# Optimization experiments

Measured on AMD Instinct MI355X. Metric: run time of the kernel, lower is better.

## Reference

```python
import jax, jax.numpy as jnp
import numpy as np

L = 32768      # sequence length
D_MODEL = 256  # input/output feature dim
D_HIDDEN = 256 # diagonal recurrent state dim
R_MIN, R_MAX, MAX_PHASE = 0.0, 1.0, 6.28


def setup_inputs() -> dict:
    key = jax.random.key(0)
    ks = jax.random.split(key, 8)
    inputs = jax.random.normal(ks[0], (L, D_MODEL), dtype=jnp.float32)
    # nu_init: log(-0.5*log(u*(r_max^2-r_min^2)+r_min^2))
    u1 = jax.random.uniform(ks[1], (D_HIDDEN,), dtype=jnp.float32)
    nu_log = jnp.log(-0.5 * jnp.log(u1 * (R_MAX**2 - R_MIN**2) + R_MIN**2))
    # theta_init: log(max_phase*u)
    u2 = jax.random.uniform(ks[2], (D_HIDDEN,), dtype=jnp.float32)
    theta_log = jnp.log(MAX_PHASE * u2)
    # gamma_log_init from (nu_log, theta_log)
    diag_lambda = jnp.exp(-jnp.exp(nu_log) + 1j * jnp.exp(theta_log))
    gamma_log = jnp.log(jnp.sqrt(1.0 - jnp.abs(diag_lambda) ** 2))
    bnorm = np.sqrt(2 * D_MODEL).astype(np.float32) if False else jnp.sqrt(2.0 * D_MODEL)
    cnorm = jnp.sqrt(2.0 * D_HIDDEN)
    B_re = jax.random.normal(ks[3], (D_HIDDEN, D_MODEL), dtype=jnp.float32) / bnorm
    B_im = jax.random.normal(ks[4], (D_HIDDEN, D_MODEL), dtype=jnp.float32) / bnorm
    C_re = jax.random.normal(ks[5], (D_MODEL, D_HIDDEN), dtype=jnp.float32) / cnorm
    C_im = jax.random.normal(ks[6], (D_MODEL, D_HIDDEN), dtype=jnp.float32) / cnorm
    D = jax.random.normal(ks[7], (D_MODEL,), dtype=jnp.float32)
    return {"inputs": inputs, "nu_log": nu_log, "theta_log": theta_log,
            "gamma_log": gamma_log, "B_re": B_re, "B_im": B_im,
            "C_re": C_re, "C_im": C_im, "D": D}


def _binop(q_i, q_j):
    # elementwise diagonal linear-recurrence combine
    A_i, b_i = q_i
    A_j, b_j = q_j
    return (A_j * A_i, A_j * b_i + b_j)


def reference(inputs, nu_log, theta_log, gamma_log, B_re, B_im, C_re, C_im, D):
    # h_{t+1} = lambda * h_t + B_norm x_{t+1};  y_t = Re[C h_t] + D * x_t
    diag_lambda = jnp.exp(-jnp.exp(nu_log) + 1j * jnp.exp(theta_log))  # (H,)
    B_norm = (B_re + 1j * B_im) * jnp.exp(gamma_log)[:, None]          # (H, M)
    C = C_re + 1j * C_im                                               # (M, H)
    Bu = inputs.astype(B_norm.dtype) @ B_norm.T                        # (L, H) complex
    Lam = jnp.broadcast_to(diag_lambda, (inputs.shape[0], diag_lambda.shape[0]))
    _, h = jax.lax.associative_scan(_binop, (Lam, Bu))                 # (L, H)
    return jnp.real(h @ C.T) + inputs * D                              # (L, M)
```

## Files before the change

kernel.cpp:

```cpp
#include <hip/hip_runtime.h>
#include <hip/hip_bf16.h>
#include <math.h>

#define LSEQ 32768
#define DMODEL 256
#define DHID 256
#define NCH 512
#define CHUNK 128
#define NCHUNKS (LSEQ / CHUNK)

typedef __bf16 bf16_t;
typedef _Float16 f16_t;
typedef __bf16 bf16x8 __attribute__((ext_vector_type(8)));
typedef float f32x4 __attribute__((ext_vector_type(4)));

__device__ __forceinline__ void async_load16(const void* g, void* l) {
  __builtin_amdgcn_global_load_lds((__attribute__((address_space(1))) void*)g,
                                   (__attribute__((address_space(3))) void*)l,
                                   16, 0, 0);
}

__device__ __forceinline__ float f16tof(unsigned int u) {
  return (float)__builtin_bit_cast(_Float16, (unsigned short)(u & 0xffffu));
}
__device__ __forceinline__ unsigned int fTobf(float f) {
  return (unsigned int)__builtin_bit_cast(unsigned short, (bf16_t)f);
}

__global__ void prep_all(const float* __restrict__ nu_log,
                         const float* __restrict__ theta_log,
                         const float* __restrict__ gamma_log,
                         const float* __restrict__ B_re, const float* __restrict__ B_im,
                         const float* __restrict__ C_re, const float* __restrict__ C_im,
                         float* __restrict__ lam, bf16_t* __restrict__ W1,
                         bf16_t* __restrict__ W2) {
  const int bid = blockIdx.x, tid = threadIdx.x;
  if (bid < 10) {
    int h = tid;
    if (h < DHID) {
      double nu = exp((double)nu_log[h]);
      double th = exp((double)theta_log[h]);
      int row; double n;
      if (bid == 0)      { row = 0; n = 1.0; }
      else if (bid == 1) { row = 2; n = 32.0; }
      else               { row = 4 + 2 * (bid - 2); n = 128.0 * (double)(1 << (bid - 2)); }
      double mag = exp(-n * nu);
      double ph  = fmod(n * th, 6.283185307179586);
      lam[row * DHID + h]       = (float)(mag * cos(ph));
      lam[(row + 1) * DHID + h] = (float)(mag * sin(ph));
    }
  } else if (bid < 522) {
    int n = bid - 10, k = tid, h = n >> 1;
    float g = expf(gamma_log[h]);
    float v = (((n & 1) == 0) ? B_re[h * DMODEL + k] : B_im[h * DMODEL + k]) * g;
    W1[n * DMODEL + k] = (bf16_t)v;
  } else {
    int idx = bid - 522;
    int m = idx >> 1, k = (idx & 1) * 256 + tid, h = k >> 1;
    float v = ((k & 1) == 0) ? C_re[m * DHID + h] : -C_im[m * DHID + h];
    W2[m * NCH + k] = (bf16_t)v;
  }
}

__global__ __launch_bounds__(512, 4) void gemm1_scan(
    const float* __restrict__ X, const bf16_t* __restrict__ Bw,
    f16_t* __restrict__ Bu, const float* __restrict__ lam,
    float* __restrict__ E) {
  __shared__ __align__(16) char smem[69632];
  char*  Bt = smem;
  float* Ep = (float*)(smem + 65536);

  const int tid = threadIdx.x;
  const int gx = blockIdx.x;
  const int c  = blockIdx.y;
  const int r0 = c * CHUNK;
  const int c0 = gx * 256;
  const int wave = tid >> 6, lane = tid & 63;
  const int wm = wave & 1, wn = wave >> 1;
  const int lrow = lane & 15, lk = lane >> 4;
  const int ra = tid >> 2, ka = (tid & 3) * 8;

  f32x4 acc[4][4] = {};

  {
    const float* xrow = X + (size_t)(r0 + ra) * DMODEL + ka;
    float4 a0 = ((const float4*)xrow)[0];
    float4 a1 = ((const float4*)xrow)[1];
    async_load16(Bw + (size_t)(c0 + ra) * DMODEL + ka, smem + 8192 + tid * 16);
    async_load16(Bw + (size_t)(c0 + 128 + ra) * DMODEL + ka, smem + 16384 + tid * 16);
    bf16x8 av = {(bf16_t)a0.x, (bf16_t)a0.y, (bf16_t)a0.z, (bf16_t)a0.w,
                 (bf16_t)a1.x, (bf16_t)a1.y, (bf16_t)a1.z, (bf16_t)a1.w};
    *(bf16x8*)(smem + ra * 64 + ka * 2) = av;
  }
  asm volatile("s_waitcnt vmcnt(0) lgkmcnt(0)" ::: "memory");
  __builtin_amdgcn_s_barrier();

#pragma unroll
  for (int t = 0; t < 8; ++t) {
    const int cur = t & 1, nxt = cur ^ 1;
    const char* Asc = smem + cur * 24576;
    const char* Bsc = smem + 8192 + cur * 24576;
    float4 a0, a1;
    if (t < 7) {
      const int k0n = (t + 1) * 32;
      const float* xrow = X + (size_t)(r0 + ra) * DMODEL + k0n + ka;
      a0 = ((const float4*)xrow)[0];
      a1 = ((const float4*)xrow)[1];
      async_load16(Bw + (size_t)(c0 + ra) * DMODEL + k0n + ka,
                   smem + 8192 + nxt * 24576 + tid * 16);
      async_load16(Bw + (size_t)(c0 + 128 + ra) * DMODEL + k0n + ka,
                   smem + 16384 + nxt * 24576 + tid * 16);
    }
    bf16x8 af[4], bfr[4];
#pragma unroll
    for (int i = 0; i < 4; ++i)
      af[i] = *(const bf16x8*)(Asc + (wm * 64 + i * 16 + lrow) * 64 + lk * 16);
#pragma unroll
    for (int j = 0; j < 4; ++j)
      bfr[j] = *(const bf16x8*)(Bsc + (wn * 64 + j * 16 + lrow) * 64 + lk * 16);
#pragma unroll
    for (int i = 0; i < 4; ++i)
#pragma unroll
      for (int j = 0; j < 4; ++j)
        acc[i][j] = __builtin_amdgcn_mfma_f32_16x16x32_bf16(af[i], bfr[j], acc[i][j], 0, 0, 0);
    if (t < 7) {
      bf16x8 av = {(bf16_t)a0.x, (bf16_t)a0.y, (bf16_t)a0.z, (bf16_t)a0.w,
                   (bf16_t)a1.x, (bf16_t)a1.y, (bf16_t)a1.z, (bf16_t)a1.w};
      *(bf16x8*)(smem + nxt * 24576 + ra * 64 + ka * 2) = av;
    }
    asm volatile("s_waitcnt vmcnt(0) lgkmcnt(0)" ::: "memory");
    __builtin_amdgcn_s_barrier();
  }

#pragma unroll
  for (int i = 0; i < 4; ++i)
#pragma unroll
    for (int r = 0; r < 4; ++r) {
      int row = wm * 64 + i * 16 + lk * 4 + r;
      int key = (row & 7) << 4;
#pragma unroll
      for (int j = 0; j < 4; ++j) {
        int col = wn * 64 + j * 16 + lrow;
        *(f16_t*)(Bt + row * 512 + ((col * 2) ^ key)) = (f16_t)acc[i][j][r];
      }
    }
  __syncthreads();

  char* dst = (char*)Bu + (size_t)r0 * 1024 + gx * 512;
#pragma unroll
  for (int it = 0; it < 8; ++it) {
    int idx = it * 512 + tid;
    int row = idx >> 5, off = (idx & 31) * 16;
    *(f32x4*)(dst + (size_t)row * 1024 + off) = *(const f32x4*)(Bt + row * 512 + off);
  }

  {
    int p = tid & 127, seg = tid >> 7;
    int h = gx * 128 + p;
    float lre = lam[h], lim = lam[DHID + h];
    float sre = 0.f, sim = 0.f;
    int cb = 4 * p;
#pragma unroll 4
    for (int t = 0; t < 32; ++t) {
      int row = seg * 32 + t;
      unsigned int w = *(const unsigned int*)(Bt + row * 512 + (cb ^ ((row & 7) << 4)));
      float bre = f16tof(w), bim = f16tof(w >> 16);
      float nre = fmaf(lre, sre, fmaf(-lim, sim, bre));
      float nim = fmaf(lre, sim, fmaf(lim, sre, bim));
      sre = nre; sim = nim;
    }
    Ep[seg * 256 + 2 * p]     = sre;
    Ep[seg * 256 + 2 * p + 1] = sim;
  }
  __syncthreads();
  if (tid < 128) {
    int p = tid, h = gx * 128 + p;
    float ar = lam[2 * DHID + h], ai = lam[3 * DHID + h];
    float er = Ep[2 * p], ei = Ep[2 * p + 1];
#pragma unroll
    for (int s = 1; s < 4; ++s) {
      float tr = fmaf(ar, er, fmaf(-ai, ei, Ep[s * 256 + 2 * p]));
      float ti = fmaf(ar, ei, fmaf(ai, er, Ep[s * 256 + 2 * p + 1]));
      er = tr; ei = ti;
    }
    E[(size_t)c * NCH + 2 * h]     = er;
    E[(size_t)c * NCH + 2 * h + 1] = ei;
  }
}

__global__ __launch_bounds__(1024) void scan_gemm2(
    const f16_t* __restrict__ Bu, const bf16_t* __restrict__ W2,
    const float* __restrict__ lam, const float* __restrict__ E,
    const float* __restrict__ X, const float* __restrict__ Dv,
    float* __restrict__ out) {
  __shared__ __align__(16) char smem[155648];
  char*   H  = smem;
  bf16_t* Bs = (bf16_t*)(smem + 131072);
  float*  LB = (float*)(smem + 131072);
  float*  Pp = (float*)(smem + 135168);
  float*  Tt = (float*)(smem + 147456);

  const int tid = threadIdx.x;
  const int c = (int)gridDim.x - 1 - (int)blockIdx.x;
  const int r0 = c * CHUNK;

  const char* src = (const char*)Bu + (size_t)r0 * 1024;
#pragma unroll
  for (int it = 0; it < 8; ++it)
    async_load16(src + it * 16384 + tid * 16, H + it * 16384 + tid * 16);

  const char* w2src = (const char*)W2 + (size_t)(tid >> 2) * (NCH * 2) + (tid & 3) * 16;
  f32x4 wreg[2];
  wreg[0] = *(const f32x4*)(w2src);

  if (tid < 512) {
    int p = tid & 255, half = tid >> 8;
    int m = c >> 1;
    int lo = half ? m : 0, end = half ? c : m;
    float aR = lam[4 * DHID + p], aI = lam[5 * DHID + p];
    float sr = 0.f, si = 0.f;
#pragma unroll 4
    for (int k = lo; k < end; ++k) {
      float2 e = *(const float2*)(E + (size_t)k * NCH + 2 * p);
      float nr = fmaf(aR, sr, fmaf(-aI, si, e.x));
      float ni = fmaf(aR, si, fmaf(aI, sr, e.y));
      sr = nr; si = ni;
    }
    LB[half * 512 + 2 * p]     = sr;
    LB[half * 512 + 2 * p + 1] = si;
  }
  __syncthreads();

  {
    int p = tid & 255, seg = tid >> 8;
    float lre = lam[p], lim = lam[DHID + p];
    float sre = 0.f, sim = 0.f;
    int cb = 4 * p;
#pragma unroll 4
    for (int t = 0; t < 32; ++t) {
      int row = seg * 32 + t;
      unsigned int w = *(const unsigned int*)(H + row * 1024 + (cb ^ ((row & 7) << 4)));
      float bre = f16tof(w), bim = f16tof(w >> 16);
      float nre = fmaf(lre, sre, fmaf(-lim, sim, bre));
      float nim = fmaf(lre, sim, fmaf(lim, sre, bim));
      sre = nre; sim = nim;
    }
    Pp[seg * 512 + 2 * p]     = sre;
    Pp[seg * 512 + 2 * p + 1] = sim;
  }
  __syncthreads();

  if (tid < 256) {
    int p = tid;
    int lenb = c - (c >> 1);
    float pr = 1.f, pi = 0.f;
#pragma unroll
    for (int j = 0; j < 8; ++j)
      if (lenb & (1 << j)) {
        float br = lam[(4 + 2 * j) * DHID + p], bi = lam[(5 + 2 * j) * DHID + p];
        float nr = pr * br - pi * bi, ni = pr * bi + pi * br;
        pr = nr; pi = ni;
      }
    float sar = LB[2 * p], sai = LB[2 * p + 1];
    float sbr = LB[512 + 2 * p], sbi = LB[512 + 2 * p + 1];
    float tr = fmaf(pr, sar, fmaf(-pi, sai, sbr));
    float ti = fmaf(pr, sai, fmaf(pi, sar, sbi));
    float l32r = lam[2 * DHID + p], l32i = lam[3 * DHID + p];
    Tt[2 * p] = tr; Tt[2 * p + 1] = ti;
#pragma unroll
    for (int s = 1; s < 4; ++s) {
      float pR = Pp[(s - 1) * 512 + 2 * p], pI = Pp[(s - 1) * 512 + 2 * p + 1];
      float nr = fmaf(l32r, tr, fmaf(-l32i, ti, pR));
      float ni = fmaf(l32r, ti, fmaf(l32i, tr, pI));
      tr = nr; ti = ni;
      Tt[s * 512 + 2 * p] = tr; Tt[s * 512 + 2 * p + 1] = ti;
    }
  }
  __syncthreads();

  {
    int p = tid & 255, seg = tid >> 8;
    float lre = lam[p], lim = lam[DHID + p];
    float sre = Tt[seg * 512 + 2 * p], sim = Tt[seg * 512 + 2 * p + 1];
    int cb = 4 * p;
#pragma unroll 4
    for (int t = 0; t < 32; ++t) {
      int row = seg * 32 + t;
      unsigned int* ptr = (unsigned int*)(H + row * 1024 + (cb ^ ((row & 7) << 4)));
      unsigned int w = *ptr;
      float bre = f16tof(w), bim = f16tof(w >> 16);
      float nre = fmaf(lre, sre, fmaf(-lim, sim, bre));
      float nim = fmaf(lre, sim, fmaf(lim, sre, bim));
      sre = nre; sim = nim;
      *ptr = (fTobf(sim) << 16) | fTobf(sre);
    }
  }
  __syncthreads();

  const int wave = tid >> 6, lane = tid & 63;
  const int wm = wave & 3, wn = wave >> 2;
  const int lrow = lane & 15, lk = lane >> 4;
  *(f32x4*)((char*)Bs + tid * 16) = wreg[0];
  wreg[1] = *(const f32x4*)(w2src + 64);
  asm volatile("s_waitcnt lgkmcnt(0)" ::: "memory");
  __builtin_amdgcn_s_barrier();

  f32x4 acc[2][4] = {};
#pragma unroll
  for (int t = 0; t < 16; ++t) {
    const int k0 = t * 32;
    bf16x8 af[2], bfr[4];
#pragma unroll
    for (int i = 0; i < 2; ++i) {
      int m = wm * 32 + i * 16 + lrow;
      af[i] = *(const bf16x8*)(H + m * 1024 + ((2 * k0 + lk * 16) ^ ((m & 7) << 4)));
    }
#pragma unroll
    for (int j = 0; j < 4; ++j)
      bfr[j] = *(const bf16x8*)(Bs + (wn * 64 + j * 16 + lrow) * 32 + lk * 8);
#pragma unroll
    for (int i = 0; i < 2; ++i)
#pragma unroll
      for (int j = 0; j < 4; ++j)
        acc[i][j] = __builtin_amdgcn_mfma_f32_16x16x32_bf16(af[i], bfr[j], acc[i][j], 0, 0, 0);
    if (t < 15) {
      __builtin_amdgcn_s_barrier();
      *(f32x4*)((char*)Bs + tid * 16) = wreg[(t + 1) & 1];
      if (t < 14) wreg[t & 1] = *(const f32x4*)(w2src + 64 * (t + 2));
      asm volatile("s_waitcnt lgkmcnt(0)" ::: "memory");
      __builtin_amdgcn_s_barrier();
    }
  }

#pragma unroll
  for (int i = 0; i < 2; ++i)
#pragma unroll
    for (int r = 0; r < 4; ++r) {
      int row = r0 + wm * 32 + i * 16 + lk * 4 + r;
#pragma unroll
      for (int j = 0; j < 4; ++j) {
        int col = wn * 64 + j * 16 + lrow;
        float v = acc[i][j][r] + X[(size_t)row * DMODEL + col] * Dv[col];
        out[(size_t)row * DMODEL + col] = v;
      }
    }
}

extern "C" void kernel_launch(void* const* d_in, const int* in_sizes, int n_in,
                              void* d_out, int out_size, void* d_ws, size_t ws_size,
                              hipStream_t stream) {
  const float* inputs    = (const float*)d_in[0];
  const float* nu_log    = (const float*)d_in[1];
  const float* theta_log = (const float*)d_in[2];
  const float* gamma_log = (const float*)d_in[3];
  const float* B_re      = (const float*)d_in[4];
  const float* B_im      = (const float*)d_in[5];
  const float* C_re      = (const float*)d_in[6];
  const float* C_im      = (const float*)d_in[7];
  const float* Dvec      = (const float*)d_in[8];
  float* out = (float*)d_out;

  char* w = (char*)d_ws;
  bf16_t* W1 = (bf16_t*)w; w += (size_t)NCH * DMODEL * 2;
  bf16_t* W2 = (bf16_t*)w; w += (size_t)DMODEL * NCH * 2;
  float* lam = (float*)w;  w += 24576;
  f16_t* Bu  = (f16_t*)w;  w += (size_t)LSEQ * NCH * 2;
  float* E   = (float*)w;  w += (size_t)NCHUNKS * NCH * 4;

  prep_all<<<1034, 256, 0, stream>>>(nu_log, theta_log, gamma_log,
                                     B_re, B_im, C_re, C_im,
                                     lam, W1, W2);
  gemm1_scan<<<dim3(2, NCHUNKS), 512, 0, stream>>>(inputs, W1, Bu, lam, E);
  scan_gemm2<<<NCHUNKS, 1024, 0, stream>>>(Bu, W2, lam, E, inputs, Dvec, out);
}
```

Before: 148.3 us.

## Triple-buffer gemm1 K loop, batch scan LDS loads, prefetch X/D in gemm2

Result: slower. 154.0 us (+3.8%).

```diff
diff --git a/kernel.cpp b/kernel.cpp
--- a/kernel.cpp
+++ b/kernel.cpp
@@ -66,9 +66,9 @@
     const float* __restrict__ X, const bf16_t* __restrict__ Bw,
     f16_t* __restrict__ Bu, const float* __restrict__ lam,
     float* __restrict__ E) {
-  __shared__ __align__(16) char smem[69632];
+  __shared__ __align__(16) char smem[77824];
   char*  Bt = smem;
-  float* Ep = (float*)(smem + 65536);
+  float* Ep = (float*)(smem + 73728);
 
   const int tid = threadIdx.x;
   const int gx = blockIdx.x;
@@ -81,35 +81,41 @@
   const int ra = tid >> 2, ka = (tid & 3) * 8;
 
   f32x4 acc[4][4] = {};
+  const float*  xbase = X + (size_t)(r0 + ra) * DMODEL + ka;
+  const bf16_t* bw0   = Bw + (size_t)(c0 + ra) * DMODEL + ka;
+  const bf16_t* bw1   = Bw + (size_t)(c0 + 128 + ra) * DMODEL + ka;
 
   {
-    const float* xrow = X + (size_t)(r0 + ra) * DMODEL + ka;
-    float4 a0 = ((const float4*)xrow)[0];
-    float4 a1 = ((const float4*)xrow)[1];
-    async_load16(Bw + (size_t)(c0 + ra) * DMODEL + ka, smem + 8192 + tid * 16);
-    async_load16(Bw + (size_t)(c0 + 128 + ra) * DMODEL + ka, smem + 16384 + tid * 16);
-    bf16x8 av = {(bf16_t)a0.x, (bf16_t)a0.y, (bf16_t)a0.z, (bf16_t)a0.w,
-                 (bf16_t)a1.x, (bf16_t)a1.y, (bf16_t)a1.z, (bf16_t)a1.w};
-    *(bf16x8*)(smem + ra * 64 + ka * 2) = av;
-  }
-  asm volatile("s_waitcnt vmcnt(0) lgkmcnt(0)" ::: "memory");
+    float4 a00 = ((const float4*)xbase)[0];
+    float4 a01 = ((const float4*)xbase)[1];
+    float4 a10 = ((const float4*)(xbase + 32))[0];
+    float4 a11 = ((const float4*)(xbase + 32))[1];
+    async_load16(bw0, smem + 8192 + tid * 16);
+    async_load16(bw1, smem + 16384 + tid * 16);
+    async_load16(bw0 + 32, smem + 24576 + 8192 + tid * 16);
+    async_load16(bw1 + 32, smem + 24576 + 16384 + tid * 16);
+    bf16x8 av0 = {(bf16_t)a00.x, (bf16_t)a00.y, (bf16_t)a00.z, (bf16_t)a00.w,
+                  (bf16_t)a01.x, (bf16_t)a01.y, (bf16_t)a01.z, (bf16_t)a01.w};
+    *(bf16x8*)(smem + ra * 64 + ka * 2) = av0;
+    bf16x8 av1 = {(bf16_t)a10.x, (bf16_t)a10.y, (bf16_t)a10.z, (bf16_t)a10.w,
+                  (bf16_t)a11.x, (bf16_t)a11.y, (bf16_t)a11.z, (bf16_t)a11.w};
+    *(bf16x8*)(smem + 24576 + ra * 64 + ka * 2) = av1;
+  }
+  asm volatile("s_waitcnt vmcnt(2) lgkmcnt(0)" ::: "memory");
   __builtin_amdgcn_s_barrier();
 
 #pragma unroll
   for (int t = 0; t < 8; ++t) {
-    const int cur = t & 1, nxt = cur ^ 1;
+    const int cur = t % 3, nx2 = (t + 2) % 3;
     const char* Asc = smem + cur * 24576;
     const char* Bsc = smem + 8192 + cur * 24576;
     float4 a0, a1;
-    if (t < 7) {
-      const int k0n = (t + 1) * 32;
-      const float* xrow = X + (size_t)(r0 + ra) * DMODEL + k0n + ka;
-      a0 = ((const float4*)xrow)[0];
-      a1 = ((const float4*)xrow)[1];
-      async_load16(Bw + (size_t)(c0 + ra) * DMODEL + k0n + ka,
-                   smem + 8192 + nxt * 24576 + tid * 16);
-      async_load16(Bw + (size_t)(c0 + 128 + ra) * DMODEL + k0n + ka,
-                   smem + 16384 + nxt * 24576 + tid * 16);
+    if (t < 6) {
+      const int k0n = (t + 2) * 32;
+      a0 = ((const float4*)(xbase + k0n))[0];
+      a1 = ((const float4*)(xbase + k0n))[1];
+      async_load16(bw0 + k0n, smem + nx2 * 24576 + 8192 + tid * 16);
+      async_load16(bw1 + k0n, smem + nx2 * 24576 + 16384 + tid * 16);
     }
     bf16x8 af[4], bfr[4];
 #pragma unroll
@@ -123,12 +129,14 @@
 #pragma unroll
       for (int j = 0; j < 4; ++j)
         acc[i][j] = __builtin_amdgcn_mfma_f32_16x16x32_bf16(af[i], bfr[j], acc[i][j], 0, 0, 0);
-    if (t < 7) {
+    if (t < 6) {
       bf16x8 av = {(bf16_t)a0.x, (bf16_t)a0.y, (bf16_t)a0.z, (bf16_t)a0.w,
                    (bf16_t)a1.x, (bf16_t)a1.y, (bf16_t)a1.z, (bf16_t)a1.w};
-      *(bf16x8*)(smem + nxt * 24576 + ra * 64 + ka * 2) = av;
-    }
-    asm volatile("s_waitcnt vmcnt(0) lgkmcnt(0)" ::: "memory");
+      *(bf16x8*)(smem + nx2 * 24576 + ra * 64 + ka * 2) = av;
+      asm volatile("s_waitcnt vmcnt(2) lgkmcnt(0)" ::: "memory");
+    } else {
+      asm volatile("s_waitcnt vmcnt(0) lgkmcnt(0)" ::: "memory");
+    }
     __builtin_amdgcn_s_barrier();
   }
 
@@ -160,14 +168,21 @@
     float lre = lam[h], lim = lam[DHID + h];
     float sre = 0.f, sim = 0.f;
     int cb = 4 * p;
-#pragma unroll 4
-    for (int t = 0; t < 32; ++t) {
-      int row = seg * 32 + t;
-      unsigned int w = *(const unsigned int*)(Bt + row * 512 + (cb ^ ((row & 7) << 4)));
-      float bre = f16tof(w), bim = f16tof(w >> 16);
-      float nre = fmaf(lre, sre, fmaf(-lim, sim, bre));
-      float nim = fmaf(lre, sim, fmaf(lim, sre, bim));
-      sre = nre; sim = nim;
+#pragma unroll
+    for (int half = 0; half < 2; ++half) {
+      unsigned int wv[16];
+#pragma unroll
+      for (int t = 0; t < 16; ++t) {
+        int row = seg * 32 + half * 16 + t;
+        wv[t] = *(const unsigned int*)(Bt + row * 512 + (cb ^ ((row & 7) << 4)));
+      }
+#pragma unroll
+      for (int t = 0; t < 16; ++t) {
+        float bre = f16tof(wv[t]), bim = f16tof(wv[t] >> 16);
+        float nre = fmaf(lre, sre, fmaf(-lim, sim, bre));
+        float nim = fmaf(lre, sim, fmaf(lim, sre, bim));
+        sre = nre; sim = nim;
+      }
     }
     Ep[seg * 256 + 2 * p]     = sre;
     Ep[seg * 256 + 2 * p + 1] = sim;
@@ -203,6 +218,9 @@
   const int tid = threadIdx.x;
   const int c = (int)gridDim.x - 1 - (int)blockIdx.x;
   const int r0 = c * CHUNK;
+  const int wave = tid >> 6, lane = tid & 63;
+  const int wm = wave & 3, wn = wave >> 2;
+  const int lrow = lane & 15, lk = lane >> 4;
 
   const char* src = (const char*)Bu + (size_t)r0 * 1024;
 #pragma unroll
@@ -212,6 +230,19 @@
   const char* w2src = (const char*)W2 + (size_t)(tid >> 2) * (NCH * 2) + (tid & 3) * 16;
   f32x4 wreg[2];
   wreg[0] = *(const f32x4*)(w2src);
+
+  float xv[32], dv[4];
+#pragma unroll
+  for (int j = 0; j < 4; ++j) dv[j] = Dv[wn * 64 + j * 16 + lrow];
+#pragma unroll
+  for (int i = 0; i < 2; ++i)
+#pragma unroll
+    for (int r = 0; r < 4; ++r) {
+      int row = r0 + wm * 32 + i * 16 + lk * 4 + r;
+#pragma unroll
+      for (int j = 0; j < 4; ++j)
+        xv[(i * 4 + r) * 4 + j] = X[(size_t)row * DMODEL + wn * 64 + j * 16 + lrow];
+    }
 
   if (tid < 512) {
     int p = tid & 255, half = tid >> 8;
@@ -236,14 +267,21 @@
     float lre = lam[p], lim = lam[DHID + p];
     float sre = 0.f, sim = 0.f;
     int cb = 4 * p;
-#pragma unroll 4
-    for (int t = 0; t < 32; ++t) {
-      int row = seg * 32 + t;
-      unsigned int w = *(const unsigned int*)(H + row * 1024 + (cb ^ ((row & 7) << 4)));
-      float bre = f16tof(w), bim = f16tof(w >> 16);
-      float nre = fmaf(lre, sre, fmaf(-lim, sim, bre));
-      float nim = fmaf(lre, sim, fmaf(lim, sre, bim));
-      sre = nre; sim = nim;
+#pragma unroll
+    for (int half = 0; half < 2; ++half) {
+      unsigned int wv[16];
+#pragma unroll
+      for (int t = 0; t < 16; ++t) {
+        int row = seg * 32 + half * 16 + t;
+        wv[t] = *(const unsigned int*)(H + row * 1024 + (cb ^ ((row & 7) << 4)));
+      }
+#pragma unroll
+      for (int t = 0; t < 16; ++t) {
+        float bre = f16tof(wv[t]), bim = f16tof(wv[t] >> 16);
+        float nre = fmaf(lre, sre, fmaf(-lim, sim, bre));
+        float nim = fmaf(lre, sim, fmaf(lim, sre, bim));
+        sre = nre; sim = nim;
+      }
     }
     Pp[seg * 512 + 2 * p]     = sre;
     Pp[seg * 512 + 2 * p + 1] = sim;
@@ -283,23 +321,28 @@
     float lre = lam[p], lim = lam[DHID + p];
     float sre = Tt[seg * 512 + 2 * p], sim = Tt[seg * 512 + 2 * p + 1];
     int cb = 4 * p;
-#pragma unroll 4
-    for (int t = 0; t < 32; ++t) {
-      int row = seg * 32 + t;
-      unsigned int* ptr = (unsigned int*)(H + row * 1024 + (cb ^ ((row & 7) << 4)));
-      unsigned int w = *ptr;
-      float bre = f16tof(w), bim = f16tof(w >> 16);
-      float nre = fmaf(lre, sre, fmaf(-lim, sim, bre));
-      float nim = fmaf(lre, sim, fmaf(lim, sre, bim));
-      sre = nre; sim = nim;
-      *ptr = (fTobf(sim) << 16) | fTobf(sre);
-    }
-  }
-  __syncthreads();
-
-  const int wave = tid >> 6, lane = tid & 63;
-  const int wm = wave & 3, wn = wave >> 2;
-  const int lrow = lane & 15, lk = lane >> 4;
+#pragma unroll
+    for (int half = 0; half < 2; ++half) {
+      unsigned int wv[16];
+#pragma unroll
+      for (int t = 0; t < 16; ++t) {
+        int row = seg * 32 + half * 16 + t;
+        wv[t] = *(const unsigned int*)(H + row * 1024 + (cb ^ ((row & 7) << 4)));
+      }
+#pragma unroll
+      for (int t = 0; t < 16; ++t) {
+        int row = seg * 32 + half * 16 + t;
+        float bre = f16tof(wv[t]), bim = f16tof(wv[t] >> 16);
+        float nre = fmaf(lre, sre, fmaf(-lim, sim, bre));
+        float nim = fmaf(lre, sim, fmaf(lim, sre, bim));
+        sre = nre; sim = nim;
+        *(unsigned int*)(H + row * 1024 + (cb ^ ((row & 7) << 4))) =
+            (fTobf(sim) << 16) | fTobf(sre);
+      }
+    }
+  }
+  __syncthreads();
+
   *(f32x4*)((char*)Bs + tid * 16) = wreg[0];
   wreg[1] = *(const f32x4*)(w2src + 64);
   asm volatile("s_waitcnt lgkmcnt(0)" ::: "memory");
@@ -340,7 +383,7 @@
 #pragma unroll
       for (int j = 0; j < 4; ++j) {
         int col = wn * 64 + j * 16 + lrow;
-        float v = acc[i][j][r] + X[(size_t)row * DMODEL + col] * Dv[col];
+        float v = acc[i][j][r] + xv[(i * 4 + r) * 4 + j] * dv[j];
         out[(size_t)row * DMODEL + col] = v;
       }
     }
```

## Use k-slab LDS layout in both GEMMs and double-buffer W2 tiles

Applied to the files above, without the earlier changes.

Result: slower. 154.8 us (+4.4%).

```diff
diff --git a/kernel.cpp b/kernel.cpp
--- a/kernel.cpp
+++ b/kernel.cpp
@@ -81,43 +81,44 @@
   const int ra = tid >> 2, ka = (tid & 3) * 8;
 
   f32x4 acc[4][4] = {};
+  const float* xbase = X + (size_t)(r0 + ra) * DMODEL + ka;
+  const int wr = tid & 255;
+  const int ws0 = (tid >> 8) * 8;
+  const int ws1 = (2 + (tid >> 8)) * 8;
+  const bf16_t* w1base = Bw + (size_t)(c0 + wr) * DMODEL;
 
   {
-    const float* xrow = X + (size_t)(r0 + ra) * DMODEL + ka;
-    float4 a0 = ((const float4*)xrow)[0];
-    float4 a1 = ((const float4*)xrow)[1];
-    async_load16(Bw + (size_t)(c0 + ra) * DMODEL + ka, smem + 8192 + tid * 16);
-    async_load16(Bw + (size_t)(c0 + 128 + ra) * DMODEL + ka, smem + 16384 + tid * 16);
+    async_load16(w1base + ws0, smem + 8192 + tid * 16);
+    async_load16(w1base + ws1, smem + 16384 + tid * 16);
+    float4 a0 = ((const float4*)xbase)[0];
+    float4 a1 = ((const float4*)xbase)[1];
     bf16x8 av = {(bf16_t)a0.x, (bf16_t)a0.y, (bf16_t)a0.z, (bf16_t)a0.w,
                  (bf16_t)a1.x, (bf16_t)a1.y, (bf16_t)a1.z, (bf16_t)a1.w};
-    *(bf16x8*)(smem + ra * 64 + ka * 2) = av;
+    *(bf16x8*)(smem + (tid & 3) * 2048 + ra * 16) = av;
   }
   asm volatile("s_waitcnt vmcnt(0) lgkmcnt(0)" ::: "memory");
   __builtin_amdgcn_s_barrier();
 
 #pragma unroll
   for (int t = 0; t < 8; ++t) {
-    const int cur = t & 1, nxt = cur ^ 1;
-    const char* Asc = smem + cur * 24576;
-    const char* Bsc = smem + 8192 + cur * 24576;
+    const int cur = t & 1;
+    const char* bufc = smem + cur * 24576;
+    char* nb = smem + (cur ^ 1) * 24576;
     float4 a0, a1;
     if (t < 7) {
       const int k0n = (t + 1) * 32;
-      const float* xrow = X + (size_t)(r0 + ra) * DMODEL + k0n + ka;
-      a0 = ((const float4*)xrow)[0];
-      a1 = ((const float4*)xrow)[1];
-      async_load16(Bw + (size_t)(c0 + ra) * DMODEL + k0n + ka,
-                   smem + 8192 + nxt * 24576 + tid * 16);
-      async_load16(Bw + (size_t)(c0 + 128 + ra) * DMODEL + k0n + ka,
-                   smem + 16384 + nxt * 24576 + tid * 16);
+      async_load16(w1base + k0n + ws0, nb + 8192 + tid * 16);
+      async_load16(w1base + k0n + ws1, nb + 16384 + tid * 16);
+      a0 = ((const float4*)(xbase + k0n))[0];
+      a1 = ((const float4*)(xbase + k0n))[1];
     }
     bf16x8 af[4], bfr[4];
 #pragma unroll
     for (int i = 0; i < 4; ++i)
-      af[i] = *(const bf16x8*)(Asc + (wm * 64 + i * 16 + lrow) * 64 + lk * 16);
+      af[i] = *(const bf16x8*)(bufc + lk * 2048 + (wm * 64 + i * 16 + lrow) * 16);
 #pragma unroll
     for (int j = 0; j < 4; ++j)
-      bfr[j] = *(const bf16x8*)(Bsc + (wn * 64 + j * 16 + lrow) * 64 + lk * 16);
+      bfr[j] = *(const bf16x8*)(bufc + 8192 + lk * 4096 + (wn * 64 + j * 16 + lrow) * 16);
 #pragma unroll
     for (int i = 0; i < 4; ++i)
 #pragma unroll
@@ -126,7 +127,7 @@
     if (t < 7) {
       bf16x8 av = {(bf16_t)a0.x, (bf16_t)a0.y, (bf16_t)a0.z, (bf16_t)a0.w,
                    (bf16_t)a1.x, (bf16_t)a1.y, (bf16_t)a1.z, (bf16_t)a1.w};
-      *(bf16x8*)(smem + nxt * 24576 + ra * 64 + ka * 2) = av;
+      *(bf16x8*)(nb + (tid & 3) * 2048 + ra * 16) = av;
     }
     asm volatile("s_waitcnt vmcnt(0) lgkmcnt(0)" ::: "memory");
     __builtin_amdgcn_s_barrier();
@@ -193,16 +194,20 @@
     const float* __restrict__ lam, const float* __restrict__ E,
     const float* __restrict__ X, const float* __restrict__ Dv,
     float* __restrict__ out) {
-  __shared__ __align__(16) char smem[155648];
+  __shared__ __align__(16) char smem[163840];
   char*   H  = smem;
-  bf16_t* Bs = (bf16_t*)(smem + 131072);
   float*  LB = (float*)(smem + 131072);
   float*  Pp = (float*)(smem + 135168);
-  float*  Tt = (float*)(smem + 147456);
+  float*  Tt = (float*)(smem + 143360);
+  char*   Bs0 = smem + 131072;
+  char*   Bs1 = smem + 147456;
 
   const int tid = threadIdx.x;
   const int c = (int)gridDim.x - 1 - (int)blockIdx.x;
   const int r0 = c * CHUNK;
+  const int wave = tid >> 6, lane = tid & 63;
+  const int wm = wave & 3, wn = wave >> 2;
+  const int lrow = lane & 15, lk = lane >> 4;
 
   const char* src = (const char*)Bu + (size_t)r0 * 1024;
 #pragma unroll
@@ -297,10 +302,7 @@
   }
   __syncthreads();
 
-  const int wave = tid >> 6, lane = tid & 63;
-  const int wm = wave & 3, wn = wave >> 2;
-  const int lrow = lane & 15, lk = lane >> 4;
-  *(f32x4*)((char*)Bs + tid * 16) = wreg[0];
+  *(f32x4*)(Bs0 + (tid & 3) * 4096 + (tid >> 2) * 16) = wreg[0];
   wreg[1] = *(const f32x4*)(w2src + 64);
   asm volatile("s_waitcnt lgkmcnt(0)" ::: "memory");
   __builtin_amdgcn_s_barrier();
@@ -309,6 +311,12 @@
 #pragma unroll
   for (int t = 0; t < 16; ++t) {
     const int k0 = t * 32;
+    const char* curb = (t & 1) ? Bs1 : Bs0;
+    char* nxtb = (t & 1) ? Bs0 : Bs1;
+    if (t < 15)
+      *(f32x4*)(nxtb + (tid & 3) * 4096 + (tid >> 2) * 16) = wreg[(t + 1) & 1];
+    if (t < 14)
+      wreg[t & 1] = *(const f32x4*)(w2src + 64 * (t + 2));
     bf16x8 af[2], bfr[4];
 #pragma unroll
     for (int i = 0; i < 2; ++i) {
@@ -317,19 +325,14 @@
     }
 #pragma unroll
     for (int j = 0; j < 4; ++j)
-      bfr[j] = *(const bf16x8*)(Bs + (wn * 64 + j * 16 + lrow) * 32 + lk * 8);
+      bfr[j] = *(const bf16x8*)(curb + lk * 4096 + (wn * 64 + j * 16 + lrow) * 16);
 #pragma unroll
     for (int i = 0; i < 2; ++i)
 #pragma unroll
       for (int j = 0; j < 4; ++j)
         acc[i][j] = __builtin_amdgcn_mfma_f32_16x16x32_bf16(af[i], bfr[j], acc[i][j], 0, 0, 0);
-    if (t < 15) {
-      __builtin_amdgcn_s_barrier();
-      *(f32x4*)((char*)Bs + tid * 16) = wreg[(t + 1) & 1];
-      if (t < 14) wreg[t & 1] = *(const f32x4*)(w2src + 64 * (t + 2));
-      asm volatile("s_waitcnt lgkmcnt(0)" ::: "memory");
-      __builtin_amdgcn_s_barrier();
-    }
+    asm volatile("s_waitcnt lgkmcnt(0)" ::: "memory");
+    __builtin_amdgcn_s_barrier();
   }
 
 #pragma unroll
```

## Load weight MFMA fragments directly from global memory instead of staging in LDS

Applied to the files above, without the earlier changes.

Result: slower. 176.7 us (+19.1%).

```diff
diff --git a/kernel.cpp b/kernel.cpp
--- a/kernel.cpp
+++ b/kernel.cpp
@@ -63,7 +63,7 @@
 }
 
 __global__ __launch_bounds__(512, 4) void gemm1_scan(
-    const float* __restrict__ X, const bf16_t* __restrict__ Bw,
+    const float* __restrict__ X, const bf16_t* __restrict__ W1,
     f16_t* __restrict__ Bu, const float* __restrict__ lam,
     float* __restrict__ E) {
   __shared__ __align__(16) char smem[69632];
@@ -81,43 +81,40 @@
   const int ra = tid >> 2, ka = (tid & 3) * 8;
 
   f32x4 acc[4][4] = {};
+  const float* xbase = X + (size_t)(r0 + ra) * DMODEL + ka;
+  const bf16_t* w1f0 = W1 + (size_t)(c0 + wn * 64 + 0 * 16 + lrow) * DMODEL + lk * 8;
+  const bf16_t* w1f1 = W1 + (size_t)(c0 + wn * 64 + 1 * 16 + lrow) * DMODEL + lk * 8;
+  const bf16_t* w1f2 = W1 + (size_t)(c0 + wn * 64 + 2 * 16 + lrow) * DMODEL + lk * 8;
+  const bf16_t* w1f3 = W1 + (size_t)(c0 + wn * 64 + 3 * 16 + lrow) * DMODEL + lk * 8;
 
   {
-    const float* xrow = X + (size_t)(r0 + ra) * DMODEL + ka;
-    float4 a0 = ((const float4*)xrow)[0];
-    float4 a1 = ((const float4*)xrow)[1];
-    async_load16(Bw + (size_t)(c0 + ra) * DMODEL + ka, smem + 8192 + tid * 16);
-    async_load16(Bw + (size_t)(c0 + 128 + ra) * DMODEL + ka, smem + 16384 + tid * 16);
+    float4 a0 = ((const float4*)xbase)[0];
+    float4 a1 = ((const float4*)xbase)[1];
     bf16x8 av = {(bf16_t)a0.x, (bf16_t)a0.y, (bf16_t)a0.z, (bf16_t)a0.w,
                  (bf16_t)a1.x, (bf16_t)a1.y, (bf16_t)a1.z, (bf16_t)a1.w};
     *(bf16x8*)(smem + ra * 64 + ka * 2) = av;
   }
-  asm volatile("s_waitcnt vmcnt(0) lgkmcnt(0)" ::: "memory");
+  asm volatile("s_waitcnt lgkmcnt(0)" ::: "memory");
   __builtin_amdgcn_s_barrier();
 
 #pragma unroll
   for (int t = 0; t < 8; ++t) {
-    const int cur = t & 1, nxt = cur ^ 1;
-    const char* Asc = smem + cur * 24576;
-    const char* Bsc = smem + 8192 + cur * 24576;
+    const char* Asc = smem + (t & 1) * 8192;
+    char* nbuf = smem + ((t + 1) & 1) * 8192;
+    const int k0 = t * 32;
     float4 a0, a1;
     if (t < 7) {
-      const int k0n = (t + 1) * 32;
-      const float* xrow = X + (size_t)(r0 + ra) * DMODEL + k0n + ka;
-      a0 = ((const float4*)xrow)[0];
-      a1 = ((const float4*)xrow)[1];
-      async_load16(Bw + (size_t)(c0 + ra) * DMODEL + k0n + ka,
-                   smem + 8192 + nxt * 24576 + tid * 16);
-      async_load16(Bw + (size_t)(c0 + 128 + ra) * DMODEL + k0n + ka,
-                   smem + 16384 + nxt * 24576 + tid * 16);
-    }
-    bf16x8 af[4], bfr[4];
+      a0 = ((const float4*)(xbase + k0 + 32))[0];
+      a1 = ((const float4*)(xbase + k0 + 32))[1];
+    }
+    bf16x8 bfr[4], af[4];
+    bfr[0] = *(const bf16x8*)(w1f0 + k0);
+    bfr[1] = *(const bf16x8*)(w1f1 + k0);
+    bfr[2] = *(const bf16x8*)(w1f2 + k0);
+    bfr[3] = *(const bf16x8*)(w1f3 + k0);
 #pragma unroll
     for (int i = 0; i < 4; ++i)
       af[i] = *(const bf16x8*)(Asc + (wm * 64 + i * 16 + lrow) * 64 + lk * 16);
-#pragma unroll
-    for (int j = 0; j < 4; ++j)
-      bfr[j] = *(const bf16x8*)(Bsc + (wn * 64 + j * 16 + lrow) * 64 + lk * 16);
 #pragma unroll
     for (int i = 0; i < 4; ++i)
 #pragma unroll
@@ -126,9 +123,9 @@
     if (t < 7) {
       bf16x8 av = {(bf16_t)a0.x, (bf16_t)a0.y, (bf16_t)a0.z, (bf16_t)a0.w,
                    (bf16_t)a1.x, (bf16_t)a1.y, (bf16_t)a1.z, (bf16_t)a1.w};
-      *(bf16x8*)(smem + nxt * 24576 + ra * 64 + ka * 2) = av;
-    }
-    asm volatile("s_waitcnt vmcnt(0) lgkmcnt(0)" ::: "memory");
+      *(bf16x8*)(nbuf + ra * 64 + ka * 2) = av;
+    }
+    asm volatile("s_waitcnt lgkmcnt(0)" ::: "memory");
     __builtin_amdgcn_s_barrier();
   }
 
@@ -193,25 +190,23 @@
     const float* __restrict__ lam, const float* __restrict__ E,
     const float* __restrict__ X, const float* __restrict__ Dv,
     float* __restrict__ out) {
-  __shared__ __align__(16) char smem[155648];
+  __shared__ __align__(16) char smem[151552];
   char*   H  = smem;
-  bf16_t* Bs = (bf16_t*)(smem + 131072);
   float*  LB = (float*)(smem + 131072);
   float*  Pp = (float*)(smem + 135168);
-  float*  Tt = (float*)(smem + 147456);
+  float*  Tt = (float*)(smem + 143360);
 
   const int tid = threadIdx.x;
   const int c = (int)gridDim.x - 1 - (int)blockIdx.x;
   const int r0 = c * CHUNK;
+  const int wave = tid >> 6, lane = tid & 63;
+  const int wm = wave & 3, wn = wave >> 2;
+  const int lrow = lane & 15, lk = lane >> 4;
 
   const char* src = (const char*)Bu + (size_t)r0 * 1024;
 #pragma unroll
   for (int it = 0; it < 8; ++it)
     async_load16(src + it * 16384 + tid * 16, H + it * 16384 + tid * 16);
-
-  const char* w2src = (const char*)W2 + (size_t)(tid >> 2) * (NCH * 2) + (tid & 3) * 16;
-  f32x4 wreg[2];
-  wreg[0] = *(const f32x4*)(w2src);
 
   if (tid < 512) {
     int p = tid & 255, half = tid >> 8;
@@ -297,39 +292,40 @@
   }
   __syncthreads();
 
-  const int wave = tid >> 6, lane = tid & 63;
-  const int wm = wave & 3, wn = wave >> 2;
-  const int lrow = lane & 15, lk = lane >> 4;
-  *(f32x4*)((char*)Bs + tid * 16) = wreg[0];
-  wreg[1] = *(const f32x4*)(w2src + 64);
-  asm volatile("s_waitcnt lgkmcnt(0)" ::: "memory");
-  __builtin_amdgcn_s_barrier();
+  const bf16_t* w2f0 = W2 + (size_t)(wn * 64 + 0 * 16 + lrow) * NCH + lk * 8;
+  const bf16_t* w2f1 = W2 + (size_t)(wn * 64 + 1 * 16 + lrow) * NCH + lk * 8;
+  const bf16_t* w2f2 = W2 + (size_t)(wn * 64 + 2 * 16 + lrow) * NCH + lk * 8;
+  const bf16_t* w2f3 = W2 + (size_t)(wn * 64 + 3 * 16 + lrow) * NCH + lk * 8;
 
   f32x4 acc[2][4] = {};
+  bf16x8 cb0 = *(const bf16x8*)(w2f0);
+  bf16x8 cb1 = *(const bf16x8*)(w2f1);
+  bf16x8 cb2 = *(const bf16x8*)(w2f2);
+  bf16x8 cb3 = *(const bf16x8*)(w2f3);
 #pragma unroll
   for (int t = 0; t < 16; ++t) {
     const int k0 = t * 32;
-    bf16x8 af[2], bfr[4];
+    bf16x8 nb0, nb1, nb2, nb3;
+    if (t < 15) {
+      nb0 = *(const bf16x8*)(w2f0 + k0 + 32);
+      nb1 = *(const bf16x8*)(w2f1 + k0 + 32);
+      nb2 = *(const bf16x8*)(w2f2 + k0 + 32);
+      nb3 = *(const bf16x8*)(w2f3 + k0 + 32);
+    }
+    bf16x8 af[2];
 #pragma unroll
     for (int i = 0; i < 2; ++i) {
       int m = wm * 32 + i * 16 + lrow;
       af[i] = *(const bf16x8*)(H + m * 1024 + ((2 * k0 + lk * 16) ^ ((m & 7) << 4)));
     }
 #pragma unroll
-    for (int j = 0; j < 4; ++j)
-      bfr[j] = *(const bf16x8*)(Bs + (wn * 64 + j * 16 + lrow) * 32 + lk * 8);
-#pragma unroll
-    for (int i = 0; i < 2; ++i)
-#pragma unroll
-      for (int j = 0; j < 4; ++j)
-        acc[i][j] = __builtin_amdgcn_mfma_f32_16x16x32_bf16(af[i], bfr[j], acc[i][j], 0, 0, 0);
-    if (t < 15) {
-      __builtin_amdgcn_s_barrier();
-      *(f32x4*)((char*)Bs + tid * 16) = wreg[(t + 1) & 1];
-      if (t < 14) wreg[t & 1] = *(const f32x4*)(w2src + 64 * (t + 2));
-      asm volatile("s_waitcnt lgkmcnt(0)" ::: "memory");
-      __builtin_amdgcn_s_barrier();
-    }
+    for (int i = 0; i < 2; ++i) {
+      acc[i][0] = __builtin_amdgcn_mfma_f32_16x16x32_bf16(af[i], cb0, acc[i][0], 0, 0, 0);
+      acc[i][1] = __builtin_amdgcn_mfma_f32_16x16x32_bf16(af[i], cb1, acc[i][1], 0, 0, 0);
+      acc[i][2] = __builtin_amdgcn_mfma_f32_16x16x32_bf16(af[i], cb2, acc[i][2], 0, 0, 0);
+      acc[i][3] = __builtin_amdgcn_mfma_f32_16x16x32_bf16(af[i], cb3, acc[i][3], 0, 0, 0);
+    }
+    if (t < 15) { cb0 = nb0; cb1 = nb1; cb2 = nb2; cb3 = nb3; }
   }
 
 #pragma unroll
```
